# Kernel tuning notes

Measured on AMD Instinct MI355X. Metric: run time of the kernel, lower is better.

The kernel has to match this reference:

```python
import jax, jax.numpy as jnp
import numpy as np

B, S, D = 2, 2048, 2048
H, DN, DR, DV = 16, 128, 64, 128   # heads, qk_nope, qk_rope, v_head
Q_LORA, KV_LORA = 1536, 512
DQ = DN + DR                        # qk_head_dim = 192
EPS = 1e-6


def setup_inputs() -> dict:
    key = jax.random.key(0)
    ks = jax.random.split(key, 8)
    s = 0.02  # weight init scale
    hidden_states = jax.random.normal(ks[0], (B, S, D), jnp.float32)
    # RoPE tables (non-interleaved HF style: cat(freqs, freqs)) per position
    inv_freq = 1.0 / (10000.0 ** (np.arange(0, DR, 2, dtype=np.float32) / DR))
    freqs = np.arange(S, dtype=np.float32)[:, None] * inv_freq[None, :]  # [S, DR/2]
    emb = np.concatenate([freqs, freqs], axis=-1)                        # [S, DR]
    cos = jnp.broadcast_to(jnp.asarray(np.cos(emb)), (B, S, DR))
    sin = jnp.broadcast_to(jnp.asarray(np.sin(emb)), (B, S, DR))
    return {
        'hidden_states': hidden_states,
        'cos': cos, 'sin': sin,
        'Wqa': jax.random.normal(ks[1], (D, Q_LORA), jnp.float32) * s,
        'qa_ln_w': jnp.ones((Q_LORA,), jnp.float32),
        'Wqb': jax.random.normal(ks[2], (Q_LORA, H * DQ), jnp.float32) * s,
        'Wkva': jax.random.normal(ks[3], (D, KV_LORA + DR), jnp.float32) * s,
        'kva_ln_w': jnp.ones((KV_LORA,), jnp.float32),
        'Wkvb': jax.random.normal(ks[4], (KV_LORA, H * (DN + DV)), jnp.float32) * s,
        'Wo': jax.random.normal(ks[5], (H * DV, D), jnp.float32) * s,
    }


def _rmsnorm(x, w):
    xf = x.astype(jnp.float32)
    var = jnp.mean(xf * xf, axis=-1, keepdims=True)
    return w * (xf * jax.lax.rsqrt(var + EPS)).astype(x.dtype)


def _rotate_half(x):
    h = x.shape[-1] // 2
    return jnp.concatenate([-x[..., h:], x[..., :h]], axis=-1)


def reference(hidden_states, cos, sin, Wqa, qa_ln_w, Wqb, Wkva, kva_ln_w, Wkvb, Wo):
    b, s, _ = hidden_states.shape
    scaling = DQ ** -0.5

    # Q path: down-proj -> RMSNorm -> up-proj -> [b, H, s, DQ]
    q = _rmsnorm(hidden_states @ Wqa, qa_ln_w) @ Wqb
    q = q.reshape(b, s, H, DQ).transpose(0, 2, 1, 3)
    q_pass, q_rot = q[..., :DN], q[..., DN:]

    # KV path: joint down-proj -> split latent / shared rope key
    ckv = hidden_states @ Wkva                       # [b, s, KV_LORA + DR]
    k_lat, k_rot = ckv[..., :KV_LORA], ckv[..., KV_LORA:]
    kv = _rmsnorm(k_lat, kva_ln_w) @ Wkvb            # [b, s, H*(DN+DV)]
    kv = kv.reshape(b, s, H, DN + DV).transpose(0, 2, 1, 3)
    k_pass, v = kv[..., :DN], kv[..., DN:]

    # decoupled RoPE on q_rot and the single shared k_rot head
    k_rot = k_rot[:, None, :, :]                     # [b, 1, s, DR]
    c, si = cos[:, None], sin[:, None]               # unsqueeze_dim=1
    q_rot = q_rot * c + _rotate_half(q_rot) * si
    k_rot = k_rot * c + _rotate_half(k_rot) * si
    k_rot = jnp.broadcast_to(k_rot, (b, H, s, DR))

    Q = jnp.concatenate([q_pass, q_rot], axis=-1)    # [b, H, s, DQ]
    K = jnp.concatenate([k_pass, k_rot], axis=-1)

    scores = jnp.einsum('bhqd,bhkd->bhqk', Q, K) * scaling
    neg = jnp.finfo(jnp.float32).min
    causal = jnp.where(jnp.tril(jnp.ones((s, s), bool)), 0.0, neg)
    scores = scores + causal
    w = jax.nn.softmax(scores.astype(jnp.float32), axis=-1).astype(Q.dtype)

    out = jnp.einsum('bhqk,bhkd->bhqd', w, v)
    out = out.transpose(0, 2, 1, 3).reshape(b, s, H * DV)
    return out @ Wo
```

## Files before the change

### kernel.cpp

```cpp
#include <hip/hip_runtime.h>
#include <math.h>

#define BB 2
#define SS 2048
#define DD 2048
#define HH 16
#define DN 128
#define DR 64
#define DV 128
#define QL 1536
#define KVL 512
#define DQ 192
#define CKVS 640
#define KVD 256
#define NCAT 2176
#define NCATP 2304
#define EPSF 1e-6f

typedef short bfrag __attribute__((ext_vector_type(8)));
typedef float facc  __attribute__((ext_vector_type(4)));

__device__ __forceinline__ ushort f2bf(float f) {
    union { float f; unsigned u; } v; v.f = f;
    unsigned r = v.u + 0x7fffu + ((v.u >> 16) & 1u);
    return (ushort)(r >> 16);
}
__device__ __forceinline__ float bf2f(ushort u) {
    union { unsigned u; float f; } v; v.u = ((unsigned)u) << 16;
    return v.f;
}
__device__ __forceinline__ float wave_red_sum(float v) {
    #pragma unroll
    for (int o = 32; o > 0; o >>= 1) v += __shfl_down(v, o);
    return v;
}
__device__ __forceinline__ void gl2lds16(const ushort* g, ushort* l) {
    __builtin_amdgcn_global_load_lds(
        (const __attribute__((address_space(1))) void*)g,
        (__attribute__((address_space(3))) void*)l, 16, 0, 0);
}
__device__ __forceinline__ void storeC(float* c, float v)  { *c = v; }
__device__ __forceinline__ void storeC(ushort* c, float v) { *c = f2bf(v); }

__global__ __launch_bounds__(256) void castf2bf(const float* __restrict__ x,
                                                ushort* __restrict__ y) {
    const int i = blockIdx.x * 256 + threadIdx.x;
    const float4 v = ((const float4*)x)[i];
    ushort4 o;
    o.x = f2bf(v.x); o.y = f2bf(v.y); o.z = f2bf(v.z); o.w = f2bf(v.w);
    ((ushort4*)y)[i] = o;
}

struct WtBatch {
    const float* src[5];
    ushort* dst[5];
    int K[5];
    int N[5];
    int nx[5];
    int base[6];
};
__global__ __launch_bounds__(256) void wtrans_b(WtBatch d) {
    __shared__ float tile[32][33];
    int bid = blockIdx.x;
    int seg = 0;
    while (bid >= d.base[seg + 1]) ++seg;
    const int l = bid - d.base[seg];
    const int nx = d.nx[seg];
    const int bx = l % nx, by = l / nx;
    const float* W = d.src[seg];
    ushort* Wt = d.dst[seg];
    const int K = d.K[seg], N = d.N[seg];
    const int k0 = by * 32, n0 = bx * 32;
    const int t = threadIdx.x;
    const int tx = t & 31, ty = t >> 5;
    #pragma unroll
    for (int r = 0; r < 4; ++r) {
        const int n = n0 + tx;
        tile[ty + r * 8][tx] =
            (n < N) ? W[(size_t)(k0 + ty + r * 8) * N + n] : 0.f;
    }
    __syncthreads();
    #pragma unroll
    for (int r = 0; r < 4; ++r) {
        const int n = n0 + ty + r * 8;
        Wt[(size_t)n * K + k0 + tx] = f2bf(tile[tx][ty + r * 8]);
    }
}


__device__ __forceinline__ void stage_half(const ushort* __restrict__ G,
                                           int ldg, int grow0, int kcol0,
                                           ushort* Lr, int wave, int lane) {
    const int r0   = lane >> 3;
    const int slot = (lane & 7) ^ r0;
    const ushort* s0 = G + (size_t)(grow0 + wave * 16 + r0) * ldg + kcol0 + slot * 8;
    gl2lds16(s0,                    Lr + wave * 1024);
    gl2lds16(s0 + (size_t)8 * ldg,  Lr + wave * 1024 + 512);
}

#define PH_PRE  do { __builtin_amdgcn_sched_barrier(0);                      \
                     __builtin_amdgcn_s_barrier();                           \
                     asm volatile("s_waitcnt lgkmcnt(0)" ::: "memory");      \
                     __builtin_amdgcn_sched_barrier(0);                      \
                     __builtin_amdgcn_s_setprio(1); } while (0)
#define PH_POST do { __builtin_amdgcn_s_setprio(0);                          \
                     __builtin_amdgcn_sched_barrier(0);                      \
                     __builtin_amdgcn_s_barrier(); } while (0)

#define MFMA16(RB)                                                           \
    _Pragma("unroll")                                                        \
    for (int i = 0; i < 4; ++i)                                              \
        _Pragma("unroll")                                                    \
        for (int j = 0; j < 4; ++j)                                          \
            acc[(RB) + i][j] = __builtin_amdgcn_mfma_f32_16x16x32_bf16(      \
                a[i], b[j], acc[(RB) + i][j], 0, 0, 0);

#define GEMM256_CORE(A_, Bt_, K_, NBX_)                                       \
    __shared__ ushort L[65536];                           \
    const int t    = threadIdx.x;                                             \
    const int lane = t & 63;                                                  \
    const int wave = t >> 6;                                                  \
    const int wm   = wave >> 2;                                               \
    const int wn   = wave & 3;                                                \
    const int quad = lane >> 4;                                               \
    const int lrow = lane & 15;                                               \
    int wg = (int)blockIdx.x;                                                 \
    { const int cpx = (int)gridDim.x >> 3; wg = (wg & 7) * cpx + (wg >> 3); } \
    const int bx = wg % (NBX_), by = wg / (NBX_);                             \
    const int m0 = by * 256, n0 = bx * 256;                                   \
    const int s0x8  = (quad ^ (lrow & 7)) * 8;       \
    const int s1x8  = s0x8 ^ 32;                   \
    const int abase = lrow * 64;                                              \
    const int bbase = (wn & 1) * 4096 + lrow * 64;                            \
    facc acc[8][4];                                                           \
    _Pragma("unroll")                                                         \
    for (int i = 0; i < 8; ++i)                                               \
        _Pragma("unroll")                                                     \
        for (int j = 0; j < 4; ++j) acc[i][j] = (facc)(0.f);                  \
    const int nk = (K_) >> 6;                                                 \
                  \
    stage_half((A_),  (K_), m0,        0, L,         wave, lane);             \
    stage_half((A_),  (K_), m0 + 128,  0, L + 8192,  wave, lane);             \
    stage_half((Bt_), (K_), n0,        0, L + 16384, wave, lane);             \
    stage_half((Bt_), (K_), n0 + 128,  0, L + 24576, wave, lane);             \
    stage_half((Bt_), (K_), n0,       64, L + 49152, wave, lane);             \
    stage_half((Bt_), (K_), n0 + 128, 64, L + 57344, wave, lane);             \
    asm volatile("s_waitcnt vmcnt(4)" ::: "memory");                          \
    __builtin_amdgcn_s_barrier();                                             \
    for (int kt = 0; kt < nk; ++kt) {                                         \
        const int p = kt & 1;                                                 \
        ushort* LA = L + p * 32768 + wm * 8192;                               \
        ushort* LB = L + p * 32768 + 16384 + (wn >> 1) * 8192;                \
        ushort* Lq = L + (p ^ 1) * 32768;                                     \
        const int kn = (kt + 1) * 64;                                         \
        bfrag a[4], b[4];                                                     \
                                           \
        _Pragma("unroll")                                                     \
        for (int i = 0; i < 4; ++i)                                           \
            a[i] = *(const bfrag*)(LA + i * 1024 + abase + s0x8);             \
        _Pragma("unroll")                                                     \
        for (int j = 0; j < 4; ++j)                                           \
            b[j] = *(const bfrag*)(LB + bbase + j * 1024 + s0x8);             \
        if (kt + 1 < nk) stage_half((A_), (K_), m0, kn, Lq, wave, lane);      \
        PH_PRE;                                                               \
        MFMA16(0)                                                             \
        PH_POST;                                                              \
                                \
        _Pragma("unroll")                                                     \
        for (int i = 0; i < 4; ++i)                                           \
            a[i] = *(const bfrag*)(LA + (4 + i) * 1024 + abase + s0x8);       \
        if (kt + 1 < nk)                                                      \
            stage_half((A_), (K_), m0 + 128, kn, Lq + 8192, wave, lane);      \
        PH_PRE;                                                               \
        MFMA16(4)                                                             \
        PH_POST;                                                              \
                                           \
        _Pragma("unroll")                                                     \
        for (int i = 0; i < 4; ++i)                                           \
            a[i] = *(const bfrag*)(LA + i * 1024 + abase + s1x8);             \
        _Pragma("unroll")                                                     \
        for (int j = 0; j < 4; ++j)                                           \
            b[j] = *(const bfrag*)(LB + bbase + j * 1024 + s1x8);             \
        PH_PRE;                                                               \
        MFMA16(0)                                                             \
        PH_POST;                                                              \
             \
        _Pragma("unroll")                                                     \
        for (int i = 0; i < 4; ++i)                                           \
            a[i] = *(const bfrag*)(LA + (4 + i) * 1024 + abase + s1x8);       \
        if (kt + 2 < nk) {                                                    \
            stage_half((Bt_), (K_), n0,       kn + 64,                        \
                       L + p * 32768 + 16384, wave, lane);                    \
            stage_half((Bt_), (K_), n0 + 128, kn + 64,                        \
                       L + p * 32768 + 24576, wave, lane);                    \
            asm volatile("s_waitcnt vmcnt(4)" ::: "memory");                  \
        } else {                                                              \
            asm volatile("s_waitcnt vmcnt(0)" ::: "memory");                  \
        }                                                                     \
        PH_PRE;                                                               \
        MFMA16(4)                                                             \
        PH_POST;                                                              \
    }

template <typename OUT, int K, int NBX, int NOUT>
__global__ __launch_bounds__(512, 2) void gemm256(const ushort* __restrict__ A,
                                                  const ushort* __restrict__ Bt,
                                                  OUT* __restrict__ C) {
    GEMM256_CORE(A, Bt, K, NBX)
    #pragma unroll
    for (int m = 0; m < 8; ++m) {
        const int row = m0 + wm * 128 + m * 16 + quad * 4;
        #pragma unroll
        for (int nf = 0; nf < 4; ++nf) {
            const int col = n0 + wn * 64 + nf * 16 + lrow;
            #pragma unroll
            for (int r = 0; r < 4; ++r)
                storeC(&C[(size_t)(row + r) * NOUT + col], acc[m][nf][r]);
        }
    }
}

__global__ __launch_bounds__(512, 2) void gemmA256(const ushort* __restrict__ A,
                                                   const ushort* __restrict__ Bt,
                                                   ushort* __restrict__ qa,
                                                   ushort* __restrict__ ckv) {
    GEMM256_CORE(A, Bt, DD, 9)
    #pragma unroll
    for (int m = 0; m < 8; ++m) {
        const int row = m0 + wm * 128 + m * 16 + quad * 4;
        #pragma unroll
        for (int nf = 0; nf < 4; ++nf) {
            const int col = n0 + wn * 64 + nf * 16 + lrow;
            #pragma unroll
            for (int r = 0; r < 4; ++r) {
                if (col < QL)
                    qa[(size_t)(row + r) * QL + col] = f2bf(acc[m][nf][r]);
                else if (col < NCAT)
                    ckv[(size_t)(row + r) * CKVS + col - QL] = f2bf(acc[m][nf][r]);
            }
        }
    }
}

__global__ __launch_bounds__(512, 2) void gemmQ256(const ushort* __restrict__ A,
                                                   const ushort* __restrict__ Bt,
                                                   ushort* __restrict__ Qbuf) {
    GEMM256_CORE(A, Bt, QL, 12)
    const float scaling = 0.07216878364870323f;
    #pragma unroll
    for (int m = 0; m < 8; ++m) {
        const int row = m0 + wm * 128 + m * 16 + quad * 4;
        #pragma unroll
        for (int nf = 0; nf < 4; ++nf) {
            const int col = n0 + wn * 64 + nf * 16 + lrow;
            const int h = col / DQ, d = col - h * DQ;
            #pragma unroll
            for (int r = 0; r < 4; ++r) {
                const int tok = row + r;
                const int b = tok >> 11, s = tok & (SS - 1);
                Qbuf[((size_t)(b * HH + h) * SS + s) * DQ + d] =
                    f2bf(acc[m][nf][r] * scaling);
            }
        }
    }
}

__global__ __launch_bounds__(256) void rmsnorm_bf_ip(ushort* __restrict__ x,
                                                     const float* __restrict__ w,
                                                     int n) {
    ushort* xr = x + (size_t)blockIdx.x * n;
    const int t = threadIdx.x;
    float ss = 0.f;
    for (int i = t; i < n; i += 256) { float v = bf2f(xr[i]); ss += v * v; }
    ss = wave_red_sum(ss);
    __shared__ float red[4];
    const int lane = t & 63, wid = t >> 6;
    if (lane == 0) red[wid] = ss;
    __syncthreads();
    const float tot = red[0] + red[1] + red[2] + red[3];
    const float scale = rsqrtf(tot / (float)n + EPSF);
    for (int i = t; i < n; i += 256) xr[i] = f2bf(w[i] * bf2f(xr[i]) * scale);
}

__global__ __launch_bounds__(256) void rmsnorm_kv(const ushort* __restrict__ x,
                                                  const float* __restrict__ w,
                                                  ushort* __restrict__ y,
                                                  ushort* __restrict__ krb,
                                                  const float* __restrict__ cosb,
                                                  const float* __restrict__ sinb) {
    const int row = blockIdx.x;
    const ushort* xr = x + (size_t)row * CKVS;
    ushort* yr = y + (size_t)row * KVL;
    const int t = threadIdx.x;
    if (t < 64) {
        const int p = t;
        const ushort* kin = xr + KVL;
        const float c  = cosb[(size_t)row * DR + p];
        const float sn = sinb[(size_t)row * DR + p];
        const float self = bf2f(kin[p]);
        const float partner = bf2f(kin[p < 32 ? p + 32 : p - 32]);
        const float v = (p < 32) ? (self * c - partner * sn)
                                 : (self * c + partner * sn);
        krb[(size_t)row * DR + p] = f2bf(v);
    }
    float ss = 0.f;
    for (int i = t; i < KVL; i += 256) { float v = bf2f(xr[i]); ss += v * v; }
    ss = wave_red_sum(ss);
    __shared__ float red[4];
    const int lane = t & 63, wid = t >> 6;
    if (lane == 0) red[wid] = ss;
    __syncthreads();
    const float tot = red[0] + red[1] + red[2] + red[3];
    const float scale = rsqrtf(tot / (float)KVL + EPSF);
    for (int i = t; i < KVL; i += 256) yr[i] = f2bf(w[i] * bf2f(xr[i]) * scale);
}

__global__ __launch_bounds__(256) void qrope(ushort* __restrict__ Qbuf,
                                             const float* __restrict__ cosb,
                                             const float* __restrict__ sinb) {
    const int tok = blockIdx.x;
    const int b = tok >> 11, s = tok & (SS - 1);
    const int t = threadIdx.x;
    const int p = t & 31, hh = t >> 5;
    const float c0 = cosb[(size_t)tok * DR + p];
    const float s0 = sinb[(size_t)tok * DR + p];
    const float c1 = cosb[(size_t)tok * DR + p + 32];
    const float s1 = sinb[(size_t)tok * DR + p + 32];
    #pragma unroll
    for (int it = 0; it < 2; ++it) {
        const int h = hh + it * 8;
        ushort* base = Qbuf + ((size_t)(b * HH + h) * SS + s) * DQ + DN;
        const float x0 = bf2f(base[p]), x1 = bf2f(base[p + 32]);
        base[p]      = f2bf(x0 * c0 - x1 * s0);
        base[p + 32] = f2bf(x1 * c1 + x0 * s1);
    }
}

__global__ __launch_bounds__(256) void vprep(const ushort* __restrict__ kv_bf,
                                             ushort* __restrict__ Vtb) {
    __shared__ ushort tile[32][33];
    const int kp0 = blockIdx.x * 32, dv0 = blockIdx.y * 32, bh = blockIdx.z;
    const int b = bh / HH, h = bh - b * HH;
    const int t = threadIdx.x, tx = t & 31, ty = t >> 5;
    #pragma unroll
    for (int r = 0; r < 4; ++r)
        tile[ty + r * 8][tx] =
            kv_bf[(size_t)(b * SS + kp0 + ty + r * 8) * (HH * KVD) + h * KVD + DN + dv0 + tx];
    __syncthreads();
    #pragma unroll
    for (int r = 0; r < 4; ++r)
        Vtb[((size_t)bh * DV + dv0 + ty + r * 8) * SS + kp0 + tx] = tile[tx][ty + r * 8];
}

__global__ __launch_bounds__(256, 2) void fattn_mfma(
    const ushort* __restrict__ Qb,
    const ushort* __restrict__ kvb,
    const ushort* __restrict__ krb,
    const ushort* __restrict__ Vt,
    ushort* __restrict__ o)
{
    const int h  = blockIdx.y;
    const int b  = blockIdx.z;
    const int qt = b ? (15 - (int)blockIdx.x) : (int)blockIdx.x;
    const int bh = b * HH + h;
    const int q0 = qt * 128;
    const int t    = threadIdx.x;
    const int lane = t & 63;
    const int wave = t >> 6;
    const int quad = lane >> 4;
    const int n    = lane & 15;
    const int wstrip = wave * 16;

    __shared__ ushort Ksu[6 * 64 * 32];
    __shared__ ushort Vtu[2 * 128 * 32];
    __shared__ ushort Psu[2 * 128 * 40];

    const ushort* vbase = Vt + (size_t)bh * DV * SS;

    bfrag aQ[2][6];
    #pragma unroll
    for (int sp = 0; sp < 2; ++sp) {
        const ushort* qrow = Qb + ((size_t)bh * SS + q0 + sp * 64 + wstrip + n) * DQ;
        #pragma unroll
        for (int kb = 0; kb < 6; ++kb)
            aQ[sp][kb] = *(const bfrag*)(qrow + kb * 32 + quad * 8);
    }

    facc oacc[2][8];
    float lp[2][4];
    #pragma unroll
    for (int sp = 0; sp < 2; ++sp) {
        #pragma unroll
        for (int jd = 0; jd < 8; ++jd) oacc[sp][jd] = (facc)(0.f);
        #pragma unroll
        for (int r = 0; r < 4; ++r) lp[sp][r] = 0.f;
    }

    #pragma unroll
    for (int i = 0; i < 6; ++i) {
        const int g = wave + 4 * i;
        const int kb = g >> 2;
        const int rem = (g & 3) * 64 + lane;
        const int row = rem >> 2, sub = rem & 3;
        const int tok = b * SS + row;
        const ushort* src = (kb < 4)
            ? kvb + (size_t)tok * (HH * KVD) + h * KVD + kb * 32 + sub * 8
            : krb + (size_t)tok * DR + (kb - 4) * 32 + sub * 8;
        gl2lds16(src, Ksu + g * 512);
    }
    #pragma unroll
    for (int i = 0; i < 4; ++i) {
        const int g = wave + 4 * i;
        const int kb2 = g >> 3;
        const int rem = (g & 7) * 64 + lane;
        const int dv = rem >> 2, sub = rem & 3;
        gl2lds16(vbase + (size_t)dv * SS + kb2 * 32 + sub * 8, Vtu + g * 512);
    }
    __syncthreads();

    const int nkt = 2 * qt + 2;
    for (int kt = 0; kt < nkt; ++kt) {
        const int k0 = kt * 64;
        const int k1 = k0 + 64;
        const bool more = (kt + 1 < nkt);

        bfrag kreg[6], vreg[4];
        if (more) {
            #pragma unroll
            for (int i = 0; i < 6; ++i) {
                const int g = wave + 4 * i;
                const int kb = g >> 2;
                const int rem = (g & 3) * 64 + lane;
                const int row = rem >> 2, sub = rem & 3;
                const int tok = b * SS + k1 + row;
                const ushort* src = (kb < 4)
                    ? kvb + (size_t)tok * (HH * KVD) + h * KVD + kb * 32 + sub * 8
                    : krb + (size_t)tok * DR + (kb - 4) * 32 + sub * 8;
                kreg[i] = *(const bfrag*)src;
            }
            #pragma unroll
            for (int i = 0; i < 4; ++i) {
                const int g = wave + 4 * i;
                const int kb2 = g >> 3;
                const int rem = (g & 7) * 64 + lane;
                const int dv = rem >> 2, sub = rem & 3;
                vreg[i] = *(const bfrag*)(vbase + (size_t)dv * SS + k1 + kb2 * 32 + sub * 8);
            }
        }

        facc s[2][4];
        #pragma unroll
        for (int sp = 0; sp < 2; ++sp)
            #pragma unroll
            for (int j = 0; j < 4; ++j) s[sp][j] = (facc)(0.f);
        #pragma unroll
        for (int kb = 0; kb < 6; ++kb) {
            #pragma unroll
            for (int j = 0; j < 4; ++j) {
                const bfrag bk =
                    *(const bfrag*)&Ksu[kb * 2048 + (j * 16 + n) * 32 + quad * 8];
                s[0][j] = __builtin_amdgcn_mfma_f32_16x16x32_bf16(aQ[0][kb], bk, s[0][j], 0, 0, 0);
                s[1][j] = __builtin_amdgcn_mfma_f32_16x16x32_bf16(aQ[1][kb], bk, s[1][j], 0, 0, 0);
            }
        }

        const bool fullt = (k1 <= q0);
        if (fullt) {
            #pragma unroll
            for (int sp = 0; sp < 2; ++sp) {
                #pragma unroll
                for (int j = 0; j < 4; ++j) {
                    #pragma unroll
                    for (int r = 0; r < 4; ++r) {
                        const float p = __expf(s[sp][j][r]);
                        lp[sp][r] += p;
                        Psu[(j >> 1) * 5120 + (sp * 64 + wstrip + quad * 4 + r) * 40
                            + (j & 1) * 16 + n] = f2bf(p);
                    }
                }
            }
        } else {
            #pragma unroll
            for (int sp = 0; sp < 2; ++sp) {
                const int rowg0 = q0 + sp * 64 + wstrip + quad * 4;
                #pragma unroll
                for (int j = 0; j < 4; ++j) {
                    const int kpos = k0 + j * 16 + n;
                    #pragma unroll
                    for (int r = 0; r < 4; ++r) {
                        const float p = (kpos <= rowg0 + r) ? __expf(s[sp][j][r]) : 0.f;
                        lp[sp][r] += p;
                        Psu[(j >> 1) * 5120 + (sp * 64 + wstrip + quad * 4 + r) * 40
                            + (j & 1) * 16 + n] = f2bf(p);
                    }
                }
            }
        }

        #pragma unroll
        for (int kb2 = 0; kb2 < 2; ++kb2) {
            const bfrag aP0 = *(const bfrag*)&Psu[kb2 * 5120 + (wstrip + n) * 40 + quad * 8];
            const bfrag aP1 = *(const bfrag*)&Psu[kb2 * 5120 + (64 + wstrip + n) * 40 + quad * 8];
            #pragma unroll
            for (int jd = 0; jd < 8; ++jd) {
                const bfrag bV = *(const bfrag*)&Vtu[kb2 * 4096 + (jd * 16 + n) * 32 + quad * 8];
                oacc[0][jd] = __builtin_amdgcn_mfma_f32_16x16x32_bf16(aP0, bV, oacc[0][jd], 0, 0, 0);
                oacc[1][jd] = __builtin_amdgcn_mfma_f32_16x16x32_bf16(aP1, bV, oacc[1][jd], 0, 0, 0);
            }
        }

        __syncthreads();
        if (more) {
            #pragma unroll
            for (int i = 0; i < 6; ++i)
                *(bfrag*)(Ksu + (wave + 4 * i) * 512 + lane * 8) = kreg[i];
            #pragma unroll
            for (int i = 0; i < 4; ++i)
                *(bfrag*)(Vtu + (wave + 4 * i) * 512 + lane * 8) = vreg[i];
        }
        __syncthreads();
    }

    #pragma unroll
    for (int sp = 0; sp < 2; ++sp) {
        #pragma unroll
        for (int r = 0; r < 4; ++r) {
            float v = lp[sp][r];
            #pragma unroll
            for (int msk = 1; msk < 16; msk <<= 1) v += __shfl_xor(v, msk);
            const float inv = 1.f / v;
            ushort* op = o + (size_t)(b * SS + q0 + sp * 64 + wstrip + quad * 4 + r)
                             * (HH * DV) + h * DV;
            #pragma unroll
            for (int jd = 0; jd < 8; ++jd)
                op[jd * 16 + n] = f2bf(oacc[sp][jd][r] * inv);
        }
    }
}

extern "C" void kernel_launch(void* const* d_in, const int* in_sizes, int n_in,
                              void* d_out, int out_size, void* d_ws, size_t ws_size,
                              hipStream_t stream) {
    const float* hs    = (const float*)d_in[0];
    const float* cosb  = (const float*)d_in[1];
    const float* sinb  = (const float*)d_in[2];
    const float* Wqa   = (const float*)d_in[3];
    const float* qa_w  = (const float*)d_in[4];
    const float* Wqb   = (const float*)d_in[5];
    const float* Wkva  = (const float*)d_in[6];
    const float* kva_w = (const float*)d_in[7];
    const float* Wkvb  = (const float*)d_in[8];
    const float* Wo    = (const float*)d_in[9];
    float* out = (float*)d_out;

    const int T = BB * SS;

    char* w = (char*)d_ws;
    auto alloc = [&](size_t bytes) {
        void* r = (void*)w;
        w += (bytes + 255) & ~(size_t)255;
        return r;
    };
    ushort* hs_bf  = (ushort*)alloc((size_t)T * DD * 2);
    ushort* Wcat   = (ushort*)alloc((size_t)NCATP * DD * 2);
    ushort* Wqbt   = (ushort*)alloc((size_t)(HH * DQ) * QL * 2);
    ushort* Wkvbt  = (ushort*)alloc((size_t)(HH * KVD) * KVL * 2);
    ushort* Wot    = (ushort*)alloc((size_t)DD * DD * 2);
    ushort* qa_bf  = (ushort*)alloc((size_t)T * QL * 2);
    ushort* Qbuf   = (ushort*)alloc((size_t)T * HH * DQ * 2);
    ushort* ckv_bf = (ushort*)alloc((size_t)T * CKVS * 2);
    ushort* kvn_bf = (ushort*)alloc((size_t)T * KVL * 2);
    ushort* kv_bf  = (ushort*)alloc((size_t)T * HH * KVD * 2);
    ushort* krb    = (ushort*)alloc((size_t)T * DR * 2);
    ushort* Vtb    = Wcat;
    ushort* ao_bf  = hs_bf;

    castf2bf<<<(T * DD / 4) / 256, 256, 0, stream>>>(hs, hs_bf);
    WtBatch wb;
    wb.src[0] = Wqa;  wb.dst[0] = Wcat;                      wb.K[0] = DD;  wb.N[0] = QL;       wb.nx[0] = 48;
    wb.src[1] = Wkva; wb.dst[1] = Wcat + (size_t)QL * DD;    wb.K[1] = DD;  wb.N[1] = KVL + DR; wb.nx[1] = 20;
    wb.src[2] = Wqb;  wb.dst[2] = Wqbt;                      wb.K[2] = QL;  wb.N[2] = HH * DQ;  wb.nx[2] = 96;
    wb.src[3] = Wkvb; wb.dst[3] = Wkvbt;                     wb.K[3] = KVL; wb.N[3] = HH * KVD; wb.nx[3] = 128;
    wb.src[4] = Wo;   wb.dst[4] = Wot;                       wb.K[4] = DD;  wb.N[4] = DD;       wb.nx[4] = 64;
    wb.base[0] = 0;
    wb.base[1] = wb.base[0] + wb.nx[0] * (DD / 32);
    wb.base[2] = wb.base[1] + wb.nx[1] * (DD / 32);
    wb.base[3] = wb.base[2] + wb.nx[2] * (QL / 32);
    wb.base[4] = wb.base[3] + wb.nx[3] * (KVL / 32);
    wb.base[5] = wb.base[4] + wb.nx[4] * (DD / 32);
    wtrans_b<<<wb.base[5], 256, 0, stream>>>(wb);

    gemmA256<<<dim3(9 * 16), 512, 0, stream>>>(hs_bf, Wcat, qa_bf, ckv_bf);
    rmsnorm_bf_ip<<<T, 256, 0, stream>>>(qa_bf, qa_w, QL);
    gemmQ256<<<dim3(12 * 16), 512, 0, stream>>>(qa_bf, Wqbt, Qbuf);
    qrope<<<T, 256, 0, stream>>>(Qbuf, cosb, sinb);
    rmsnorm_kv<<<T, 256, 0, stream>>>(ckv_bf, kva_w, kvn_bf, krb, cosb, sinb);
    gemm256<ushort, KVL, 16, HH * KVD><<<dim3(16 * 16), 512, 0, stream>>>(kvn_bf, Wkvbt, kv_bf);
    vprep<<<dim3(SS / 32, DV / 32, BB * HH), 256, 0, stream>>>(kv_bf, Vtb);
    fattn_mfma<<<dim3(16, HH, BB), 256, 0, stream>>>(Qbuf, kv_bf, krb, Vtb, ao_bf);
    gemm256<float, DD, 8, DD><<<dim3(8 * 16), 512, 0, stream>>>(ao_bf, Wot, out);
}
```

Measured before the change: 449.0 us.

## Add 256x128 output GEMM, fold log2e into Q scale, use raw exp2 in attention

Replaces the final output projection GEMM (256x256 tiles, 128 blocks) with a new 256x128-tile kernel launching 256 blocks, with a triple-buffered B stage and XCD-aware block remapping, so that more of the GPU's compute units are busy. Folds log2(e) into the Q scaling constant so softmax can call the hardware v_exp_f32 (exp2) directly instead of __expf. Also adds a sched_barrier after the K/V register loads in the attention loop to control instruction scheduling. The exp2 change relies on the scale constant being exactly log2e times the original, and the new GEMM adds more code that has to be kept correct.

After: 430.1 us. -4.2%, faster.

```diff
diff --git a/kernel.cpp b/kernel.cpp
--- a/kernel.cpp
+++ b/kernel.cpp
@@ -28,6 +28,9 @@
 __device__ __forceinline__ float bf2f(ushort u) {
     union { unsigned u; float f; } v; v.u = ((unsigned)u) << 16;
     return v.f;
+}
+__device__ __forceinline__ float fexp2(float x) {
+    float r; asm("v_exp_f32 %0, %1" : "=v"(r) : "v"(x)); return r;
 }
 __device__ __forceinline__ float wave_red_sum(float v) {
     #pragma unroll
@@ -220,6 +223,82 @@
     }
 }
 
+template <int K, int NBX, int NOUT>
+__global__ __launch_bounds__(512, 2) void gemmW(const ushort* __restrict__ A,
+                                                const ushort* __restrict__ Bt,
+                                                float* __restrict__ C) {
+    __shared__ ushort L[57344];
+    const int t    = threadIdx.x;
+    const int lane = t & 63;
+    const int wave = t >> 6;
+    const int wm   = wave >> 1;
+    const int wn   = wave & 1;
+    const int quad = lane >> 4;
+    const int lrow = lane & 15;
+    int wg = (int)blockIdx.x;
+    { const int cpx = (int)gridDim.x >> 3; wg = (wg & 7) * cpx + (wg >> 3); }
+    const int bx = wg % NBX, by = wg / NBX;
+    const int m0 = by * 256, n0 = bx * 128;
+    const int s0x8 = (quad ^ (lrow & 7)) * 8;
+    const int s1x8 = s0x8 ^ 32;
+    facc acc[4][4];
+    #pragma unroll
+    for (int i = 0; i < 4; ++i)
+        #pragma unroll
+        for (int j = 0; j < 4; ++j) acc[i][j] = (facc)(0.f);
+    const int nk = K >> 6;
+    stage_half(A,  K, m0,        0, L,          wave, lane);
+    stage_half(A,  K, m0 + 128,  0, L + 8192,   wave, lane);
+    stage_half(Bt, K, n0,        0, L + 32768,  wave, lane);
+    stage_half(Bt, K, n0,       64, L + 40960,  wave, lane);
+    asm volatile("s_waitcnt vmcnt(0)" ::: "memory");
+    __builtin_amdgcn_s_barrier();
+    int bp = 0, bp2 = 2;
+    for (int kt = 0; kt < nk; ++kt) {
+        const int p = kt & 1;
+        ushort* LA = L + p * 16384 + (wm >> 1) * 8192
+                       + ((wm & 1) * 64 + lrow) * 64;
+        ushort* LB = L + 32768 + bp * 8192 + (wn * 64 + lrow) * 64;
+        const int kn = (kt + 1) * 64;
+        bfrag a[4], b[4];
+        #pragma unroll
+        for (int i = 0; i < 4; ++i) a[i] = *(const bfrag*)(LA + i * 1024 + s0x8);
+        #pragma unroll
+        for (int j = 0; j < 4; ++j) b[j] = *(const bfrag*)(LB + j * 1024 + s0x8);
+        if (kt + 1 < nk) {
+            stage_half(A, K, m0,       kn, L + (p ^ 1) * 16384,        wave, lane);
+            stage_half(A, K, m0 + 128, kn, L + (p ^ 1) * 16384 + 8192, wave, lane);
+        }
+        if (kt + 2 < nk)
+            stage_half(Bt, K, n0, kn + 64, L + 32768 + bp2 * 8192, wave, lane);
+        PH_PRE;
+        MFMA16(0)
+        PH_POST;
+        #pragma unroll
+        for (int i = 0; i < 4; ++i) a[i] = *(const bfrag*)(LA + i * 1024 + s1x8);
+        #pragma unroll
+        for (int j = 0; j < 4; ++j) b[j] = *(const bfrag*)(LB + j * 1024 + s1x8);
+        if (kt + 2 < nk) { asm volatile("s_waitcnt vmcnt(2)" ::: "memory"); }
+        else             { asm volatile("s_waitcnt vmcnt(0)" ::: "memory"); }
+        PH_PRE;
+        MFMA16(0)
+        PH_POST;
+        bp  = (bp  == 2) ? 0 : bp  + 1;
+        bp2 = (bp2 == 2) ? 0 : bp2 + 1;
+    }
+    #pragma unroll
+    for (int m = 0; m < 4; ++m) {
+        const int row = m0 + wm * 64 + m * 16 + quad * 4;
+        #pragma unroll
+        for (int nf = 0; nf < 4; ++nf) {
+            const int col = n0 + wn * 64 + nf * 16 + lrow;
+            #pragma unroll
+            for (int r = 0; r < 4; ++r)
+                C[(size_t)(row + r) * NOUT + col] = acc[m][nf][r];
+        }
+    }
+}
+
 __global__ __launch_bounds__(512, 2) void gemmA256(const ushort* __restrict__ A,
                                                    const ushort* __restrict__ Bt,
                                                    ushort* __restrict__ qa,
@@ -246,7 +325,7 @@
                                                    const ushort* __restrict__ Bt,
                                                    ushort* __restrict__ Qbuf) {
     GEMM256_CORE(A, Bt, QL, 12)
-    const float scaling = 0.07216878364870323f;
+    const float scaling = 0.10411754831f;
     #pragma unroll
     for (int m = 0; m < 8; ++m) {
         const int row = m0 + wm * 128 + m * 16 + quad * 4;
@@ -447,6 +526,7 @@
                 vreg[i] = *(const bfrag*)(vbase + (size_t)dv * SS + k1 + kb2 * 32 + sub * 8);
             }
         }
+        __builtin_amdgcn_sched_barrier(0);
 
         facc s[2][4];
         #pragma unroll
@@ -472,7 +552,7 @@
                 for (int j = 0; j < 4; ++j) {
                     #pragma unroll
                     for (int r = 0; r < 4; ++r) {
-                        const float p = __expf(s[sp][j][r]);
+                        const float p = fexp2(s[sp][j][r]);
                         lp[sp][r] += p;
                         Psu[(j >> 1) * 5120 + (sp * 64 + wstrip + quad * 4 + r) * 40
                             + (j & 1) * 16 + n] = f2bf(p);
@@ -488,7 +568,7 @@
                     const int kpos = k0 + j * 16 + n;
                     #pragma unroll
                     for (int r = 0; r < 4; ++r) {
-                        const float p = (kpos <= rowg0 + r) ? __expf(s[sp][j][r]) : 0.f;
+                        const float p = (kpos <= rowg0 + r) ? fexp2(s[sp][j][r]) : 0.f;
                         lp[sp][r] += p;
                         Psu[(j >> 1) * 5120 + (sp * 64 + wstrip + quad * 4 + r) * 40
                             + (j & 1) * 16 + n] = f2bf(p);
@@ -598,5 +678,5 @@
     gemm256<ushort, KVL, 16, HH * KVD><<<dim3(16 * 16), 512, 0, stream>>>(kvn_bf, Wkvbt, kv_bf);
     vprep<<<dim3(SS / 32, DV / 32, BB * HH), 256, 0, stream>>>(kv_bf, Vtb);
     fattn_mfma<<<dim3(16, HH, BB), 256, 0, stream>>>(Qbuf, kv_bf, krb, Vtb, ao_bf);
-    gemm256<float, DD, 8, DD><<<dim3(8 * 16), 512, 0, stream>>>(ao_bf, Wot, out);
-}
+    gemmW<DD, 16, DD><<<dim3(256), 512, 0, stream>>>(ao_bf, Wot, out);
+}
```
